# Performance work log

Measured on AMD Instinct MI355X. Metric: run time of the kernel, lower is better.

Reference implementation:

```python
import jax, jax.numpy as jnp
import numpy as np

N = 131072      # total nodes
B = 16          # graphs in batch (num_segments)
C = 128         # in_channels
K = 16          # n_super_nodes
TAU = 1.0
PRUNING_THRESHOLD = 0.01
SPARSITY_WEIGHT = 0.01
TEMPORAL_W = 0.1 * 5
COLLAPSE_W = 2.0
EPS = 1e-9


def setup_inputs() -> dict:
    key = jax.random.key(0)
    ks = jax.random.split(key, 8)
    x = jax.random.normal(ks[0], (N, C), dtype=jnp.float32)
    batch = jnp.sort(jax.random.randint(ks[1], (N,), 0, B)).astype(jnp.int64)
    pos = jax.random.normal(ks[2], (N, 2), dtype=jnp.float32)
    # Gumbel noise for gumbel_softmax (sampled once, passed as input for determinism)
    gumbel = jax.random.gumbel(ks[3], (N, K), dtype=jnp.float32)
    # assign_mlp params: Linear(C,C) -> ReLU -> Linear(C,K)
    W1 = jax.random.normal(ks[4], (C, C), dtype=jnp.float32) / np.sqrt(C)
    b1 = jnp.zeros((C,), dtype=jnp.float32)
    W2 = jax.random.normal(ks[5], (K, C), dtype=jnp.float32) / np.sqrt(C)
    b2 = jnp.zeros((K,), dtype=jnp.float32)
    scaling = jnp.asarray(10.0, dtype=jnp.float32)
    active_mask = jnp.ones((K,), dtype=jnp.float32)  # buffer, starts all-active
    return {"x": x, "batch": batch, "pos": pos, "gumbel": gumbel,
            "W1": W1, "b1": b1, "W2": W2, "b2": b2,
            "scaling": scaling, "active_mask": active_mask}


def reference(x, batch, pos, gumbel, W1, b1, W2, b2, scaling, active_mask):
    # --- assignment logits: MLP * scaling (eval mode, prev_assignments=None) ---
    h = jax.nn.relu(x @ W1.T + b1)            # [N, C]
    logits = (h @ W2.T + b2) * scaling        # [N, K]
    # eval-path masking: masked_fill(mask == 0, -1e9)
    masked_logits = jnp.where(active_mask[None, :] == 0.0, -1e9, logits)
    # gumbel_softmax (soft, hard=False)
    s = jax.nn.softmax((masked_logits + gumbel) / TAU, axis=-1)   # [N, K]

    avg_s = jnp.mean(s, axis=0)               # [K]

    # --- losses ---
    entropy = -jnp.mean(jnp.sum(s * jnp.log(s + EPS), axis=1))
    uniform_p = 1.0 / K
    diversity = jnp.sum(uniform_p * jnp.log(uniform_p / (avg_s + EPS)))
    pruning = jnp.mean(jnp.abs(avg_s * (1.0 - active_mask)))
    sparsity = (jnp.sum(active_mask) / K) * SPARSITY_WEIGHT
    temporal = jnp.asarray(0.0, jnp.float32)  # prev_assignments is None
    # collapse-prevention / balance bodies are truncated upstream; faithful proxies
    collapse = jnp.sum((avg_s - uniform_p) ** 2) * COLLAPSE_W
    balance = jnp.std(avg_s)
    spatial = jnp.asarray(0.0, jnp.float32)

    # --- pooled features: out[b,k,c] = sum_{n in graph b} s[n,k] * x[n,c] ---
    weighted = x[:, None, :] * s[:, :, None]                  # [N, K, C]
    out = jax.ops.segment_sum(weighted, batch, num_segments=B)  # [B, K, C]

    # --- super-node positions ---
    w_pos = pos[:, None, :] * s[:, :, None]                    # [N, K, 2]
    sum_s_pos = jax.ops.segment_sum(w_pos, batch, num_segments=B)  # [B, K, 2]
    sum_s = jax.ops.segment_sum(s, batch, num_segments=B)[..., None] + EPS  # [B, K, 1]
    mu = sum_s_pos / sum_s                                     # [B, K, 2]

    # --- separation loss: pairwise repulsion between super-node centers ---
    dist_sq = jnp.sum((mu[:, :, None, :] - mu[:, None, :, :]) ** 2, axis=-1)  # [B,K,K]
    eye = jnp.eye(K, dtype=mu.dtype)[None]
    repulsion = 1.0 / (dist_sq + 1.0)
    separation = jnp.sum(repulsion * (1.0 - eye)) / (K * (K - 1))

    losses = jnp.stack([entropy, diversity, spatial, pruning, sparsity,
                        temporal * TEMPORAL_W, collapse, balance, separation])
    return out, s, mu, losses
```

## Files before the change

### kernel.cpp

```cpp
#include <hip/hip_runtime.h>
#include <hip/hip_bf16.h>
#include <math.h>

#define NN 131072
#define BSEG 16
#define CCH 128
#define KK 16
#define EPSF 1e-9f
#define XST 136

#define OFF_S   32768
#define OFF_MU  2129920
#define OFF_L   2130432

#define REDC_BASE 1024
#define REDC_STRIDE 1024
#define NRED 64
#define ST_BASE (REDC_BASE + NRED * REDC_STRIDE)
#define NST 4
#define ST_SZ (BSEG * KK * CCH)

typedef __bf16 bf16x8 __attribute__((ext_vector_type(8)));
typedef float  f32x4  __attribute__((ext_vector_type(4)));
typedef float  f32x16 __attribute__((ext_vector_type(16)));

__device__ __forceinline__ int load_batch(const void* bptr, int n, int is64) {
    if (is64) return (int)((const long long*)bptr)[n];
    return ((const int*)bptr)[n];
}

__device__ __forceinline__ float wave_sum(float v) {
#pragma unroll
    for (int o = 32; o > 0; o >>= 1) v += __shfl_xor(v, o, 64);
    return v;
}

__device__ __forceinline__ bf16x8 pack8(float4 a, float4 b) {
    bf16x8 v;
    v[0] = (__bf16)a.x; v[1] = (__bf16)a.y; v[2] = (__bf16)a.z; v[3] = (__bf16)a.w;
    v[4] = (__bf16)b.x; v[5] = (__bf16)b.y; v[6] = (__bf16)b.z; v[7] = (__bf16)b.w;
    return v;
}

__global__ void k_zero(float* __restrict__ ws, const int* __restrict__ b32) {
    int i = blockIdx.x * 256 + threadIdx.x;
    ws[REDC_BASE + i] = 0.0f;
    if (i == 0) ws[0] = (b32[NN - 1] == 0) ? 1.0f : 0.0f;
}

__global__ __launch_bounds__(256, 2) void k_fused(
    const float* __restrict__ x, const void* __restrict__ batch,
    const float* __restrict__ pos, const float* __restrict__ gumbel,
    const float* __restrict__ W1, const float* __restrict__ b1,
    const float* __restrict__ W2, const float* __restrict__ b2,
    const float* __restrict__ scaling, const float* __restrict__ active_mask,
    float* __restrict__ s_out, float* __restrict__ ws)
{
    __shared__ __align__(16) __bf16 x_lds[128 * XST];
    __shared__ __align__(16) __bf16 h_lds[128 * XST];
    __shared__ __align__(16) __bf16 sT[16 * XST];
    __shared__ int bsegs[128];

    const int tid  = threadIdx.x;
    const int lane = tid & 63;
    const int wv   = tid >> 6;
    const int n0   = blockIdx.x * 128;
    const int is64 = (int)ws[0];

    if (tid < 128) bsegs[tid] = load_batch(batch, n0 + tid, is64);

    float4 ga0, ga1, ga2, ga3;
    if (tid < 128) {
        const float4* gp = (const float4*)(gumbel + (size_t)(n0 + tid) * KK);
        ga0 = gp[0]; ga1 = gp[1]; ga2 = gp[2]; ga3 = gp[3];
    }

    {
        const float4* xg = (const float4*)(x + (size_t)n0 * CCH);
#pragma unroll
        for (int i = 0; i < 8; i++) {
            int p = i * 256 + tid;
            float4 a = xg[2 * p], b = xg[2 * p + 1];
            *(bf16x8*)&x_lds[(p >> 4) * XST + (p & 15) * 8] = pack8(a, b);
        }
    }
    __syncthreads();

    {
        bf16x8 bfr[8];
        const float* wrow = W1 + (size_t)(wv * 32 + (lane & 31)) * CCH + (lane >> 5) * 8;
#pragma unroll
        for (int ks = 0; ks < 8; ks++) {
            float4 u = *(const float4*)(wrow + ks * 16);
            float4 v = *(const float4*)(wrow + ks * 16 + 4);
            bfr[ks] = pack8(u, v);
        }
        f32x16 acc[4];
#pragma unroll
        for (int mt = 0; mt < 4; mt++)
#pragma unroll
            for (int r = 0; r < 16; r++) acc[mt][r] = 0.0f;

#pragma unroll
        for (int ks = 0; ks < 8; ks++) {
#pragma unroll
            for (int mt = 0; mt < 4; mt++) {
                bf16x8 a = *(bf16x8*)&x_lds[(size_t)(mt * 32 + (lane & 31)) * XST + ks * 16 + (lane >> 5) * 8];
                acc[mt] = __builtin_amdgcn_mfma_f32_32x32x16_bf16(a, bfr[ks], acc[mt], 0, 0, 0);
            }
        }
        const float b1j = b1[wv * 32 + (lane & 31)];
#pragma unroll
        for (int mt = 0; mt < 4; mt++)
#pragma unroll
            for (int r = 0; r < 16; r++) {
                int node = mt * 32 + (r & 3) + 8 * (r >> 2) + 4 * (lane >> 5);
                h_lds[(size_t)node * XST + wv * 32 + (lane & 31)] = (__bf16)fmaxf(acc[mt][r] + b1j, 0.0f);
            }
    }
    __syncthreads();

    {
        f32x4 acc2[2];
#pragma unroll
        for (int t = 0; t < 2; t++)
#pragma unroll
            for (int r = 0; r < 4; r++) acc2[t][r] = 0.0f;

#pragma unroll
        for (int ks = 0; ks < 4; ks++) {
            const float* w2row = W2 + (size_t)(lane & 15) * CCH + ks * 32 + (lane >> 4) * 8;
            float4 u = *(const float4*)w2row;
            float4 v = *(const float4*)(w2row + 4);
            bf16x8 bw = pack8(u, v);
#pragma unroll
            for (int t = 0; t < 2; t++) {
                int tile = wv * 2 + t;
                bf16x8 a = *(bf16x8*)&h_lds[(size_t)(tile * 16 + (lane & 15)) * XST + ks * 32 + (lane >> 4) * 8];
                acc2[t] = __builtin_amdgcn_mfma_f32_16x16x32_bf16(a, bw, acc2[t], 0, 0, 0);
            }
        }
#pragma unroll
        for (int t = 0; t < 2; t++) {
#pragma unroll
            for (int r = 0; r < 4; r++) {
                int node = (wv * 2 + t) * 16 + (lane >> 4) * 4 + r;
                float* lp = (float*)((char*)h_lds + (size_t)node * (XST * 2) + 192);
                lp[lane & 15] = acc2[t][r];
            }
        }
    }
    __syncthreads();

    if (tid < 128) {
        const int n = n0 + tid;
        const char* rb = (const char*)h_lds + (size_t)tid * (XST * 2);
        float lg[16], gu[16];
#pragma unroll
        for (int i = 0; i < 4; i++) {
            float4 t = *(const float4*)(rb + 192 + 16 * i);
            lg[4 * i] = t.x; lg[4 * i + 1] = t.y; lg[4 * i + 2] = t.z; lg[4 * i + 3] = t.w;
        }
        gu[0] = ga0.x; gu[1] = ga0.y; gu[2]  = ga0.z; gu[3]  = ga0.w;
        gu[4] = ga1.x; gu[5] = ga1.y; gu[6]  = ga1.z; gu[7]  = ga1.w;
        gu[8] = ga2.x; gu[9] = ga2.y; gu[10] = ga2.z; gu[11] = ga2.w;
        gu[12] = ga3.x; gu[13] = ga3.y; gu[14] = ga3.z; gu[15] = ga3.w;

        const float sc = scaling[0];
        float m = -1e30f;
#pragma unroll
        for (int k = 0; k < KK; k++) {
            float v = (lg[k] + b2[k]) * sc;
            if (active_mask[k] == 0.0f) v = -1e9f;
            v += gu[k];
            lg[k] = v;
            m = fmaxf(m, v);
        }
        float ssum = 0.0f;
#pragma unroll
        for (int k = 0; k < KK; k++) { lg[k] = expf(lg[k] - m); ssum += lg[k]; }
        const float inv = 1.0f / ssum;
        float sarr[16];
#pragma unroll
        for (int k = 0; k < KK; k++) sarr[k] = lg[k] * inv;

        float4* srow = (float4*)(s_out + (size_t)n * KK);
#pragma unroll
        for (int i = 0; i < 4; i++) {
            float4 t;
            t.x = sarr[4 * i]; t.y = sarr[4 * i + 1]; t.z = sarr[4 * i + 2]; t.w = sarr[4 * i + 3];
            srow[i] = t;
        }
#pragma unroll
        for (int k = 0; k < KK; k++) sT[k * XST + tid] = (__bf16)sarr[k];

        float ent = 0.0f;
#pragma unroll
        for (int k = 0; k < KK; k++) ent += sarr[k] * logf(sarr[k] + EPSF);

        const float2 p = ((const float2*)pos)[n];
        const int bi = bsegs[tid];
        const int b0 = __shfl(bi, 0, 64);
        const int b1s = __shfl(bi, 63, 64);
        const float prim = (bi == b0) ? 1.0f : 0.0f;
        float* rc = ws + REDC_BASE + (size_t)(blockIdx.x & (NRED - 1)) * REDC_STRIDE;

#pragma unroll
        for (int k = 0; k < KK; k++) {
            float v = wave_sum(sarr[k] * prim);
            if (lane == 0) atomicAdd(&rc[b0 * 16 + k], v);
        }
#pragma unroll
        for (int k = 0; k < KK; k++) {
            float vx = wave_sum(sarr[k] * p.x * prim);
            float vy = wave_sum(sarr[k] * p.y * prim);
            if (lane == 0) {
                atomicAdd(&rc[256 + b0 * 32 + 2 * k],     vx);
                atomicAdd(&rc[256 + b0 * 32 + 2 * k + 1], vy);
            }
        }
        {
            float e = wave_sum(ent * prim);
            if (lane == 0) atomicAdd(&rc[768], e);
        }

        if (b0 != b1s) {
            const float sec = 1.0f - prim;
#pragma unroll
            for (int k = 0; k < KK; k++) {
                float v = wave_sum(sarr[k] * sec);
                if (lane == 0) atomicAdd(&rc[b1s * 16 + k], v);
            }
#pragma unroll
            for (int k = 0; k < KK; k++) {
                float vx = wave_sum(sarr[k] * p.x * sec);
                float vy = wave_sum(sarr[k] * p.y * sec);
                if (lane == 0) {
                    atomicAdd(&rc[256 + b1s * 32 + 2 * k],     vx);
                    atomicAdd(&rc[256 + b1s * 32 + 2 * k + 1], vy);
                }
            }
            float e = wave_sum(ent * sec);
            if (lane == 0) atomicAdd(&rc[768], e);
        }
    }
    __syncthreads();

    {
        float* stg = ws + ST_BASE + (size_t)(blockIdx.x & (NST - 1)) * ST_SZ;
        const int bfirst = bsegs[0], blast = bsegs[127];
        for (int seg = bfirst; seg <= blast; seg++) {
            const bool masked = (bfirst != blast);
            f32x4 pacc[2];
#pragma unroll
            for (int t = 0; t < 2; t++)
#pragma unroll
                for (int r = 0; r < 4; r++) pacc[t][r] = 0.0f;

#pragma unroll
            for (int ks = 0; ks < 4; ks++) {
                bf16x8 a = *(bf16x8*)&sT[(size_t)(lane & 15) * XST + ks * 32 + (lane >> 4) * 8];
                if (masked) {
#pragma unroll
                    for (int i = 0; i < 8; i++) {
                        int nd = ks * 32 + (lane >> 4) * 8 + i;
                        if (bsegs[nd] != seg) a[i] = (__bf16)0.0f;
                    }
                }
#pragma unroll
                for (int t = 0; t < 2; t++) {
                    int ct = wv * 2 + t;
                    bf16x8 bx;
#pragma unroll
                    for (int i = 0; i < 8; i++)
                        bx[i] = x_lds[(size_t)(ks * 32 + (lane >> 4) * 8 + i) * XST + ct * 16 + (lane & 15)];
                    pacc[t] = __builtin_amdgcn_mfma_f32_16x16x32_bf16(a, bx, pacc[t], 0, 0, 0);
                }
            }
#pragma unroll
            for (int t = 0; t < 2; t++) {
                int c = (wv * 2 + t) * 16 + (lane & 15);
#pragma unroll
                for (int r = 0; r < 4; r++) {
                    int k = (lane >> 4) * 4 + r;
                    atomicAdd(&stg[((size_t)seg * KK + k) * CCH + c], pacc[t][r]);
                }
            }
        }
    }
}

__global__ __launch_bounds__(256) void k_reduce(const float* __restrict__ ws,
                                                float* __restrict__ out) {
    int i = blockIdx.x * 256 + threadIdx.x;
    const float4* s0 = (const float4*)(ws + ST_BASE);
    const float4* s1 = (const float4*)(ws + ST_BASE + ST_SZ);
    const float4* s2 = (const float4*)(ws + ST_BASE + 2 * ST_SZ);
    const float4* s3 = (const float4*)(ws + ST_BASE + 3 * ST_SZ);
    float4 a = s0[i], b = s1[i], c = s2[i], d = s3[i];
    float4 r;
    r.x = (a.x + b.x) + (c.x + d.x);
    r.y = (a.y + b.y) + (c.y + d.y);
    r.z = (a.z + b.z) + (c.z + d.z);
    r.w = (a.w + b.w) + (c.w + d.w);
    ((float4*)out)[i] = r;
}

__global__ __launch_bounds__(256) void k_final(
    const float* __restrict__ ws, const float* __restrict__ active_mask,
    float* __restrict__ mu_out, float* __restrict__ losses)
{
    __shared__ float lsum[256];
    __shared__ float lpos[512];
    __shared__ float lent[1];
    __shared__ float smu[512];
    __shared__ float savg[16];
    __shared__ float red[256];
    const int tid = threadIdx.x;

    for (int a = tid; a < 769; a += 256) {
        float acc = 0.0f;
#pragma unroll 8
        for (int c = 0; c < NRED; c++) acc += ws[REDC_BASE + c * REDC_STRIDE + a];
        if (a < 256) lsum[a] = acc;
        else if (a < 768) lpos[a - 256] = acc;
        else lent[0] = acc;
    }
    __syncthreads();

    if (tid < 16) {
        float a = 0.0f;
#pragma unroll
        for (int b = 0; b < 16; b++) a += lsum[b * 16 + tid];
        savg[tid] = a / (float)NN;
    }
    for (int i = tid; i < 512; i += 256) {
        int sk = i >> 1;
        float v = lpos[i] / (lsum[sk] + EPSF);
        smu[i] = v;
        mu_out[i] = v;
    }
    __syncthreads();

    float rep = 0.0f;
    for (int t = tid; t < 4096; t += 256) {
        int b = t >> 8, i = (t >> 4) & 15, j = t & 15;
        if (i != j) {
            float dx = smu[b * 32 + i * 2]     - smu[b * 32 + j * 2];
            float dy = smu[b * 32 + i * 2 + 1] - smu[b * 32 + j * 2 + 1];
            rep += 1.0f / (dx * dx + dy * dy + 1.0f);
        }
    }
    red[tid] = rep;
    __syncthreads();
    for (int st = 128; st > 0; st >>= 1) {
        if (tid < st) red[tid] += red[tid + st];
        __syncthreads();
    }

    if (tid == 0) {
        const float p = 1.0f / 16.0f;
        float separation = red[0] / (float)(16 * 15);
        float entropy = -lent[0] / (float)NN;
        float diversity = 0.f, pruning = 0.f, amsum = 0.f, collapse = 0.f, mean = 0.f;
        for (int k = 0; k < 16; k++) {
            float a = savg[k];
            diversity += p * logf(p / (a + EPSF));
            pruning += fabsf(a * (1.0f - active_mask[k]));
            amsum += active_mask[k];
            collapse += (a - p) * (a - p);
            mean += a;
        }
        pruning /= 16.0f;
        mean /= 16.0f;
        float var = 0.f;
        for (int k = 0; k < 16; k++) { float d = savg[k] - mean; var += d * d; }
        float balance = sqrtf(var / 16.0f);
        float sparsity = (amsum / 16.0f) * 0.01f;
        collapse *= 2.0f;
        losses[0] = entropy;   losses[1] = diversity; losses[2] = 0.0f;
        losses[3] = pruning;   losses[4] = sparsity;  losses[5] = 0.0f;
        losses[6] = collapse;  losses[7] = balance;   losses[8] = separation;
    }
}

extern "C" void kernel_launch(void* const* d_in, const int* in_sizes, int n_in,
                              void* d_out, int out_size, void* d_ws, size_t ws_size,
                              hipStream_t stream) {
    const float* x       = (const float*)d_in[0];
    const void*  batch   = d_in[1];
    const float* pos     = (const float*)d_in[2];
    const float* gumbel  = (const float*)d_in[3];
    const float* W1      = (const float*)d_in[4];
    const float* b1      = (const float*)d_in[5];
    const float* W2      = (const float*)d_in[6];
    const float* b2      = (const float*)d_in[7];
    const float* scaling = (const float*)d_in[8];
    const float* am      = (const float*)d_in[9];

    float* out      = (float*)d_out;
    float* s_sec    = out + OFF_S;
    float* mu_sec   = out + OFF_MU;
    float* loss_sec = out + OFF_L;
    float* wsf      = (float*)d_ws;

    k_zero<<<768, 256, 0, stream>>>(wsf, (const int*)batch);
    k_fused<<<NN / 128, 256, 0, stream>>>(x, batch, pos, gumbel, W1, b1, W2, b2,
                                          scaling, am, s_sec, wsf);
    k_reduce<<<32, 256, 0, stream>>>(wsf, out);
    k_final<<<1, 256, 0, stream>>>(wsf, am, mu_sec, loss_sec);
}
```

Baseline: 183.0 us.

## Use 512-thread blocks over two node tiles, carry pooled accumulators, merge tail kernels

Each block now has 8 waves and walks two consecutive 128-node tiles, so there are half as many blocks. W1 fragments are loaded once per block and reused across both tiles. The pooled-feature MFMA accumulator is carried across tiles and flushed with atomics only when the segment changes, which cuts global atomic traffic. The reduce and final kernels are merged into one launch to remove a kernel launch. The costs are more barriers per block, per-wave work split differently (one 16-column tile per wave), and occupancy limited by LDS at 512 threads.

```diff
diff --git a/kernel.cpp b/kernel.cpp
--- a/kernel.cpp
+++ b/kernel.cpp
@@ -20,6 +20,8 @@
 #define NST 4
 #define ST_SZ (BSEG * KK * CCH)
 
+#define TILES 2
+
 typedef __bf16 bf16x8 __attribute__((ext_vector_type(8)));
 typedef float  f32x4  __attribute__((ext_vector_type(4)));
 typedef float  f32x16 __attribute__((ext_vector_type(16)));
@@ -48,7 +50,7 @@
     if (i == 0) ws[0] = (b32[NN - 1] == 0) ? 1.0f : 0.0f;
 }
 
-__global__ __launch_bounds__(256, 2) void k_fused(
+__global__ __launch_bounds__(512, 4) void k_fused(
     const float* __restrict__ x, const void* __restrict__ batch,
     const float* __restrict__ pos, const float* __restrict__ gumbel,
     const float* __restrict__ W1, const float* __restrict__ b1,
@@ -64,259 +66,269 @@
     const int tid  = threadIdx.x;
     const int lane = tid & 63;
     const int wv   = tid >> 6;
-    const int n0   = blockIdx.x * 128;
     const int is64 = (int)ws[0];
 
-    if (tid < 128) bsegs[tid] = load_batch(batch, n0 + tid, is64);
-
-    float4 ga0, ga1, ga2, ga3;
-    if (tid < 128) {
-        const float4* gp = (const float4*)(gumbel + (size_t)(n0 + tid) * KK);
-        ga0 = gp[0]; ga1 = gp[1]; ga2 = gp[2]; ga3 = gp[3];
-    }
-
+    const int c0 = (wv & 3) * 32;
+    bf16x8 bfr[8];
     {
-        const float4* xg = (const float4*)(x + (size_t)n0 * CCH);
-#pragma unroll
-        for (int i = 0; i < 8; i++) {
-            int p = i * 256 + tid;
-            float4 a = xg[2 * p], b = xg[2 * p + 1];
-            *(bf16x8*)&x_lds[(p >> 4) * XST + (p & 15) * 8] = pack8(a, b);
-        }
-    }
-    __syncthreads();
-
-    {
-        bf16x8 bfr[8];
-        const float* wrow = W1 + (size_t)(wv * 32 + (lane & 31)) * CCH + (lane >> 5) * 8;
+        const float* wrow = W1 + (size_t)(c0 + (lane & 31)) * CCH + (lane >> 5) * 8;
 #pragma unroll
         for (int ks = 0; ks < 8; ks++) {
             float4 u = *(const float4*)(wrow + ks * 16);
             float4 v = *(const float4*)(wrow + ks * 16 + 4);
             bfr[ks] = pack8(u, v);
         }
-        f32x16 acc[4];
-#pragma unroll
-        for (int mt = 0; mt < 4; mt++)
-#pragma unroll
-            for (int r = 0; r < 16; r++) acc[mt][r] = 0.0f;
-
-#pragma unroll
-        for (int ks = 0; ks < 8; ks++) {
-#pragma unroll
-            for (int mt = 0; mt < 4; mt++) {
-                bf16x8 a = *(bf16x8*)&x_lds[(size_t)(mt * 32 + (lane & 31)) * XST + ks * 16 + (lane >> 5) * 8];
-                acc[mt] = __builtin_amdgcn_mfma_f32_32x32x16_bf16(a, bfr[ks], acc[mt], 0, 0, 0);
-            }
-        }
-        const float b1j = b1[wv * 32 + (lane & 31)];
-#pragma unroll
-        for (int mt = 0; mt < 4; mt++)
-#pragma unroll
-            for (int r = 0; r < 16; r++) {
-                int node = mt * 32 + (r & 3) + 8 * (r >> 2) + 4 * (lane >> 5);
-                h_lds[(size_t)node * XST + wv * 32 + (lane & 31)] = (__bf16)fmaxf(acc[mt][r] + b1j, 0.0f);
-            }
-    }
-    __syncthreads();
-
-    {
-        f32x4 acc2[2];
-#pragma unroll
-        for (int t = 0; t < 2; t++)
-#pragma unroll
-            for (int r = 0; r < 4; r++) acc2[t][r] = 0.0f;
-
-#pragma unroll
-        for (int ks = 0; ks < 4; ks++) {
-            const float* w2row = W2 + (size_t)(lane & 15) * CCH + ks * 32 + (lane >> 4) * 8;
-            float4 u = *(const float4*)w2row;
-            float4 v = *(const float4*)(w2row + 4);
-            bf16x8 bw = pack8(u, v);
-#pragma unroll
-            for (int t = 0; t < 2; t++) {
-                int tile = wv * 2 + t;
-                bf16x8 a = *(bf16x8*)&h_lds[(size_t)(tile * 16 + (lane & 15)) * XST + ks * 32 + (lane >> 4) * 8];
-                acc2[t] = __builtin_amdgcn_mfma_f32_16x16x32_bf16(a, bw, acc2[t], 0, 0, 0);
-            }
-        }
-#pragma unroll
-        for (int t = 0; t < 2; t++) {
+    }
+    const float b1j = b1[c0 + (lane & 31)];
+
+    f32x4 pacc;
+#pragma unroll
+    for (int r = 0; r < 4; r++) pacc[r] = 0.0f;
+    int curseg = -1;
+    float* rc  = ws + REDC_BASE + (size_t)(blockIdx.x & (NRED - 1)) * REDC_STRIDE;
+    float* stg = ws + ST_BASE   + (size_t)(blockIdx.x & (NST  - 1)) * ST_SZ;
+
+    for (int t = 0; t < TILES; t++) {
+        const int n0 = blockIdx.x * (TILES * 128) + t * 128;
+
+        if (t) __syncthreads();
+
+        if (tid < 128) bsegs[tid] = load_batch(batch, n0 + tid, is64);
+
+        float4 ga0, ga1, ga2, ga3;
+        float2 p;
+        if (tid < 128) {
+            const float4* gp = (const float4*)(gumbel + (size_t)(n0 + tid) * KK);
+            ga0 = gp[0]; ga1 = gp[1]; ga2 = gp[2]; ga3 = gp[3];
+            p = ((const float2*)pos)[n0 + tid];
+        }
+
+        {
+            const float4* xg = (const float4*)(x + (size_t)n0 * CCH);
+#pragma unroll
+            for (int i = 0; i < 4; i++) {
+                int pp = i * 512 + tid;
+                float4 a = xg[2 * pp], b = xg[2 * pp + 1];
+                *(bf16x8*)&x_lds[(pp >> 4) * XST + (pp & 15) * 8] = pack8(a, b);
+            }
+        }
+        __syncthreads();
+
+        {
+            f32x16 acc[2];
+#pragma unroll
+            for (int m = 0; m < 2; m++)
+#pragma unroll
+                for (int r = 0; r < 16; r++) acc[m][r] = 0.0f;
+
+            const int mt0 = (wv >> 2) * 2;
+#pragma unroll
+            for (int ks = 0; ks < 8; ks++) {
+#pragma unroll
+                for (int m = 0; m < 2; m++) {
+                    bf16x8 a = *(bf16x8*)&x_lds[(size_t)((mt0 + m) * 32 + (lane & 31)) * XST + ks * 16 + (lane >> 5) * 8];
+                    acc[m] = __builtin_amdgcn_mfma_f32_32x32x16_bf16(a, bfr[ks], acc[m], 0, 0, 0);
+                }
+            }
+#pragma unroll
+            for (int m = 0; m < 2; m++)
+#pragma unroll
+                for (int r = 0; r < 16; r++) {
+                    int node = (mt0 + m) * 32 + (r & 3) + 8 * (r >> 2) + 4 * (lane >> 5);
+                    h_lds[(size_t)node * XST + c0 + (lane & 31)] = (__bf16)fmaxf(acc[m][r] + b1j, 0.0f);
+                }
+        }
+        __syncthreads();
+
+        {
+            f32x4 acc2;
+#pragma unroll
+            for (int r = 0; r < 4; r++) acc2[r] = 0.0f;
+#pragma unroll
+            for (int ks = 0; ks < 4; ks++) {
+                const float* w2row = W2 + (size_t)(lane & 15) * CCH + ks * 32 + (lane >> 4) * 8;
+                float4 u = *(const float4*)w2row;
+                float4 v = *(const float4*)(w2row + 4);
+                bf16x8 bwf = pack8(u, v);
+                bf16x8 a = *(bf16x8*)&h_lds[(size_t)(wv * 16 + (lane & 15)) * XST + ks * 32 + (lane >> 4) * 8];
+                acc2 = __builtin_amdgcn_mfma_f32_16x16x32_bf16(a, bwf, acc2, 0, 0, 0);
+            }
 #pragma unroll
             for (int r = 0; r < 4; r++) {
-                int node = (wv * 2 + t) * 16 + (lane >> 4) * 4 + r;
+                int node = wv * 16 + (lane >> 4) * 4 + r;
                 float* lp = (float*)((char*)h_lds + (size_t)node * (XST * 2) + 192);
-                lp[lane & 15] = acc2[t][r];
-            }
-        }
-    }
-    __syncthreads();
-
-    if (tid < 128) {
-        const int n = n0 + tid;
-        const char* rb = (const char*)h_lds + (size_t)tid * (XST * 2);
-        float lg[16], gu[16];
-#pragma unroll
-        for (int i = 0; i < 4; i++) {
-            float4 t = *(const float4*)(rb + 192 + 16 * i);
-            lg[4 * i] = t.x; lg[4 * i + 1] = t.y; lg[4 * i + 2] = t.z; lg[4 * i + 3] = t.w;
-        }
-        gu[0] = ga0.x; gu[1] = ga0.y; gu[2]  = ga0.z; gu[3]  = ga0.w;
-        gu[4] = ga1.x; gu[5] = ga1.y; gu[6]  = ga1.z; gu[7]  = ga1.w;
-        gu[8] = ga2.x; gu[9] = ga2.y; gu[10] = ga2.z; gu[11] = ga2.w;
-        gu[12] = ga3.x; gu[13] = ga3.y; gu[14] = ga3.z; gu[15] = ga3.w;
-
-        const float sc = scaling[0];
-        float m = -1e30f;
-#pragma unroll
-        for (int k = 0; k < KK; k++) {
-            float v = (lg[k] + b2[k]) * sc;
-            if (active_mask[k] == 0.0f) v = -1e9f;
-            v += gu[k];
-            lg[k] = v;
-            m = fmaxf(m, v);
-        }
-        float ssum = 0.0f;
-#pragma unroll
-        for (int k = 0; k < KK; k++) { lg[k] = expf(lg[k] - m); ssum += lg[k]; }
-        const float inv = 1.0f / ssum;
-        float sarr[16];
-#pragma unroll
-        for (int k = 0; k < KK; k++) sarr[k] = lg[k] * inv;
-
-        float4* srow = (float4*)(s_out + (size_t)n * KK);
-#pragma unroll
-        for (int i = 0; i < 4; i++) {
-            float4 t;
-            t.x = sarr[4 * i]; t.y = sarr[4 * i + 1]; t.z = sarr[4 * i + 2]; t.w = sarr[4 * i + 3];
-            srow[i] = t;
-        }
-#pragma unroll
-        for (int k = 0; k < KK; k++) sT[k * XST + tid] = (__bf16)sarr[k];
-
-        float ent = 0.0f;
-#pragma unroll
-        for (int k = 0; k < KK; k++) ent += sarr[k] * logf(sarr[k] + EPSF);
-
-        const float2 p = ((const float2*)pos)[n];
-        const int bi = bsegs[tid];
-        const int b0 = __shfl(bi, 0, 64);
-        const int b1s = __shfl(bi, 63, 64);
-        const float prim = (bi == b0) ? 1.0f : 0.0f;
-        float* rc = ws + REDC_BASE + (size_t)(blockIdx.x & (NRED - 1)) * REDC_STRIDE;
-
-#pragma unroll
-        for (int k = 0; k < KK; k++) {
-            float v = wave_sum(sarr[k] * prim);
-            if (lane == 0) atomicAdd(&rc[b0 * 16 + k], v);
-        }
-#pragma unroll
-        for (int k = 0; k < KK; k++) {
-            float vx = wave_sum(sarr[k] * p.x * prim);
-            float vy = wave_sum(sarr[k] * p.y * prim);
-            if (lane == 0) {
-                atomicAdd(&rc[256 + b0 * 32 + 2 * k],     vx);
-                atomicAdd(&rc[256 + b0 * 32 + 2 * k + 1], vy);
-            }
-        }
+                lp[lane & 15] = acc2[r];
+            }
+        }
+        __syncthreads();
+
+        if (tid < 128) {
+            const int n = n0 + tid;
+            const char* rb = (const char*)h_lds + (size_t)tid * (XST * 2);
+            float lg[16], gu[16];
+#pragma unroll
+            for (int i = 0; i < 4; i++) {
+                float4 tt = *(const float4*)(rb + 192 + 16 * i);
+                lg[4 * i] = tt.x; lg[4 * i + 1] = tt.y; lg[4 * i + 2] = tt.z; lg[4 * i + 3] = tt.w;
+            }
+            gu[0] = ga0.x; gu[1] = ga0.y; gu[2]  = ga0.z; gu[3]  = ga0.w;
+            gu[4] = ga1.x; gu[5] = ga1.y; gu[6]  = ga1.z; gu[7]  = ga1.w;
+            gu[8] = ga2.x; gu[9] = ga2.y; gu[10] = ga2.z; gu[11] = ga2.w;
+            gu[12] = ga3.x; gu[13] = ga3.y; gu[14] = ga3.z; gu[15] = ga3.w;
+
+            const float sc = scaling[0];
+            float m = -1e30f;
+#pragma unroll
+            for (int k = 0; k < KK; k++) {
+                float v = (lg[k] + b2[k]) * sc;
+                if (active_mask[k] == 0.0f) v = -1e9f;
+                v += gu[k];
+                lg[k] = v;
+                m = fmaxf(m, v);
+            }
+            float ssum = 0.0f;
+#pragma unroll
+            for (int k = 0; k < KK; k++) { lg[k] = expf(lg[k] - m); ssum += lg[k]; }
+            const float inv = 1.0f / ssum;
+            float sarr[16];
+#pragma unroll
+            for (int k = 0; k < KK; k++) sarr[k] = lg[k] * inv;
+
+            float4* srow = (float4*)(s_out + (size_t)n * KK);
+#pragma unroll
+            for (int i = 0; i < 4; i++) {
+                float4 tt;
+                tt.x = sarr[4 * i]; tt.y = sarr[4 * i + 1]; tt.z = sarr[4 * i + 2]; tt.w = sarr[4 * i + 3];
+                srow[i] = tt;
+            }
+#pragma unroll
+            for (int k = 0; k < KK; k++) sT[k * XST + tid] = (__bf16)sarr[k];
+
+            float ent = 0.0f;
+#pragma unroll
+            for (int k = 0; k < KK; k++) ent += sarr[k] * logf(sarr[k] + EPSF);
+
+            const int bi = bsegs[tid];
+            const int b0 = __shfl(bi, 0, 64);
+            const int b1s = __shfl(bi, 63, 64);
+            const float prim = (bi == b0) ? 1.0f : 0.0f;
+
+#pragma unroll
+            for (int k = 0; k < KK; k++) {
+                float v = wave_sum(sarr[k] * prim);
+                if (lane == 0) atomicAdd(&rc[b0 * 16 + k], v);
+            }
+#pragma unroll
+            for (int k = 0; k < KK; k++) {
+                float vx = wave_sum(sarr[k] * p.x * prim);
+                float vy = wave_sum(sarr[k] * p.y * prim);
+                if (lane == 0) {
+                    atomicAdd(&rc[256 + b0 * 32 + 2 * k],     vx);
+                    atomicAdd(&rc[256 + b0 * 32 + 2 * k + 1], vy);
+                }
+            }
+            {
+                float e = wave_sum(ent * prim);
+                if (lane == 0) atomicAdd(&rc[768], e);
+            }
+
+            if (b0 != b1s) {
+                const float sec = 1.0f - prim;
+#pragma unroll
+                for (int k = 0; k < KK; k++) {
+                    float v = wave_sum(sarr[k] * sec);
+                    if (lane == 0) atomicAdd(&rc[b1s * 16 + k], v);
+                }
+#pragma unroll
+                for (int k = 0; k < KK; k++) {
+                    float vx = wave_sum(sarr[k] * p.x * sec);
+                    float vy = wave_sum(sarr[k] * p.y * sec);
+                    if (lane == 0) {
+                        atomicAdd(&rc[256 + b1s * 32 + 2 * k],     vx);
+                        atomicAdd(&rc[256 + b1s * 32 + 2 * k + 1], vy);
+                    }
+                }
+                float e = wave_sum(ent * sec);
+                if (lane == 0) atomicAdd(&rc[768], e);
+            }
+        }
+        __syncthreads();
+
         {
-            float e = wave_sum(ent * prim);
-            if (lane == 0) atomicAdd(&rc[768], e);
-        }
-
-        if (b0 != b1s) {
-            const float sec = 1.0f - prim;
-#pragma unroll
-            for (int k = 0; k < KK; k++) {
-                float v = wave_sum(sarr[k] * sec);
-                if (lane == 0) atomicAdd(&rc[b1s * 16 + k], v);
-            }
-#pragma unroll
-            for (int k = 0; k < KK; k++) {
-                float vx = wave_sum(sarr[k] * p.x * sec);
-                float vy = wave_sum(sarr[k] * p.y * sec);
-                if (lane == 0) {
-                    atomicAdd(&rc[256 + b1s * 32 + 2 * k],     vx);
-                    atomicAdd(&rc[256 + b1s * 32 + 2 * k + 1], vy);
-                }
-            }
-            float e = wave_sum(ent * sec);
-            if (lane == 0) atomicAdd(&rc[768], e);
-        }
-    }
-    __syncthreads();
-
-    {
-        float* stg = ws + ST_BASE + (size_t)(blockIdx.x & (NST - 1)) * ST_SZ;
-        const int bfirst = bsegs[0], blast = bsegs[127];
-        for (int seg = bfirst; seg <= blast; seg++) {
-            const bool masked = (bfirst != blast);
-            f32x4 pacc[2];
-#pragma unroll
-            for (int t = 0; t < 2; t++)
-#pragma unroll
-                for (int r = 0; r < 4; r++) pacc[t][r] = 0.0f;
-
-#pragma unroll
-            for (int ks = 0; ks < 4; ks++) {
-                bf16x8 a = *(bf16x8*)&sT[(size_t)(lane & 15) * XST + ks * 32 + (lane >> 4) * 8];
-                if (masked) {
-#pragma unroll
-                    for (int i = 0; i < 8; i++) {
-                        int nd = ks * 32 + (lane >> 4) * 8 + i;
-                        if (bsegs[nd] != seg) a[i] = (__bf16)0.0f;
+            const int bf = bsegs[0], bl = bsegs[127];
+            const bool masked = (bf != bl);
+            for (int seg = bf; seg <= bl; seg++) {
+                if (seg != curseg) {
+                    if (curseg >= 0) {
+#pragma unroll
+                        for (int r = 0; r < 4; r++) {
+                            int k = (lane >> 4) * 4 + r;
+                            int c = wv * 16 + (lane & 15);
+                            atomicAdd(&stg[((size_t)curseg * KK + k) * CCH + c], pacc[r]);
+                        }
+#pragma unroll
+                        for (int r = 0; r < 4; r++) pacc[r] = 0.0f;
                     }
-                }
-#pragma unroll
-                for (int t = 0; t < 2; t++) {
-                    int ct = wv * 2 + t;
+                    curseg = seg;
+                }
+#pragma unroll
+                for (int ks = 0; ks < 4; ks++) {
+                    bf16x8 a = *(bf16x8*)&sT[(size_t)(lane & 15) * XST + ks * 32 + (lane >> 4) * 8];
+                    if (masked) {
+#pragma unroll
+                        for (int i = 0; i < 8; i++) {
+                            int nd = ks * 32 + (lane >> 4) * 8 + i;
+                            if (bsegs[nd] != seg) a[i] = (__bf16)0.0f;
+                        }
+                    }
                     bf16x8 bx;
 #pragma unroll
                     for (int i = 0; i < 8; i++)
-                        bx[i] = x_lds[(size_t)(ks * 32 + (lane >> 4) * 8 + i) * XST + ct * 16 + (lane & 15)];
-                    pacc[t] = __builtin_amdgcn_mfma_f32_16x16x32_bf16(a, bx, pacc[t], 0, 0, 0);
-                }
-            }
-#pragma unroll
-            for (int t = 0; t < 2; t++) {
-                int c = (wv * 2 + t) * 16 + (lane & 15);
-#pragma unroll
-                for (int r = 0; r < 4; r++) {
-                    int k = (lane >> 4) * 4 + r;
-                    atomicAdd(&stg[((size_t)seg * KK + k) * CCH + c], pacc[t][r]);
-                }
-            }
-        }
-    }
-}
-
-__global__ __launch_bounds__(256) void k_reduce(const float* __restrict__ ws,
-                                                float* __restrict__ out) {
-    int i = blockIdx.x * 256 + threadIdx.x;
-    const float4* s0 = (const float4*)(ws + ST_BASE);
-    const float4* s1 = (const float4*)(ws + ST_BASE + ST_SZ);
-    const float4* s2 = (const float4*)(ws + ST_BASE + 2 * ST_SZ);
-    const float4* s3 = (const float4*)(ws + ST_BASE + 3 * ST_SZ);
-    float4 a = s0[i], b = s1[i], c = s2[i], d = s3[i];
-    float4 r;
-    r.x = (a.x + b.x) + (c.x + d.x);
-    r.y = (a.y + b.y) + (c.y + d.y);
-    r.z = (a.z + b.z) + (c.z + d.z);
-    r.w = (a.w + b.w) + (c.w + d.w);
-    ((float4*)out)[i] = r;
-}
-
-__global__ __launch_bounds__(256) void k_final(
+                        bx[i] = x_lds[(size_t)(ks * 32 + (lane >> 4) * 8 + i) * XST + wv * 16 + (lane & 15)];
+                    pacc = __builtin_amdgcn_mfma_f32_16x16x32_bf16(a, bx, pacc, 0, 0, 0);
+                }
+            }
+        }
+    }
+
+    if (curseg >= 0) {
+#pragma unroll
+        for (int r = 0; r < 4; r++) {
+            int k = (lane >> 4) * 4 + r;
+            int c = wv * 16 + (lane & 15);
+            atomicAdd(&stg[((size_t)curseg * KK + k) * CCH + c], pacc[r]);
+        }
+    }
+}
+
+__global__ __launch_bounds__(256) void k_tail(
     const float* __restrict__ ws, const float* __restrict__ active_mask,
-    float* __restrict__ mu_out, float* __restrict__ losses)
+    float* __restrict__ out, float* __restrict__ mu_out, float* __restrict__ losses)
 {
+    const int tid = threadIdx.x;
+
+    if (blockIdx.x < 32) {
+        int i = blockIdx.x * 256 + tid;
+        const float4* s0 = (const float4*)(ws + ST_BASE);
+        const float4* s1 = (const float4*)(ws + ST_BASE + ST_SZ);
+        const float4* s2 = (const float4*)(ws + ST_BASE + 2 * ST_SZ);
+        const float4* s3 = (const float4*)(ws + ST_BASE + 3 * ST_SZ);
+        float4 a = s0[i], b = s1[i], c = s2[i], d = s3[i];
+        float4 r;
+        r.x = (a.x + b.x) + (c.x + d.x);
+        r.y = (a.y + b.y) + (c.y + d.y);
+        r.z = (a.z + b.z) + (c.z + d.z);
+        r.w = (a.w + b.w) + (c.w + d.w);
+        ((float4*)out)[i] = r;
+        return;
+    }
+
     __shared__ float lsum[256];
     __shared__ float lpos[512];
     __shared__ float lent[1];
     __shared__ float smu[512];
     __shared__ float savg[16];
     __shared__ float red[256];
-    const int tid = threadIdx.x;
 
     for (int a = tid; a < 769; a += 256) {
         float acc = 0.0f;
@@ -405,8 +417,7 @@
     float* wsf      = (float*)d_ws;
 
     k_zero<<<768, 256, 0, stream>>>(wsf, (const int*)batch);
-    k_fused<<<NN / 128, 256, 0, stream>>>(x, batch, pos, gumbel, W1, b1, W2, b2,
+    k_fused<<<NN / 256, 512, 0, stream>>>(x, batch, pos, gumbel, W1, b1, W2, b2,
                                           scaling, am, s_sec, wsf);
-    k_reduce<<<32, 256, 0, stream>>>(wsf, out);
-    k_final<<<1, 256, 0, stream>>>(wsf, am, mu_sec, loss_sec);
-}
+    k_tail<<<33, 256, 0, stream>>>(wsf, am, out, mu_sec, loss_sec);
+}
```

After: 215.4 us. 17.7% more time.

## Compute softmax in MFMA register layout and merge reduce/final kernels

Applied to the files above, without the earlier changes.

The gumbel softmax, entropy and segment sums now run directly on the second-MFMA accumulator layout across all 256 threads. Row max and sum use 16-lane shuffles, which removes the LDS round trip of logits, one barrier, and the per-k wave reductions that only half the block performed. Per-segment sums are accumulated per lane and reduced once before the atomics, cutting the atomic count. The separate reduce and final kernels are merged into one 33-block launch to save a kernel launch. In exchange, s is written to global memory as scattered scalar stores instead of float4 rows.

```diff
diff --git a/kernel.cpp b/kernel.cpp
--- a/kernel.cpp
+++ b/kernel.cpp
@@ -59,6 +59,7 @@
     __shared__ __align__(16) __bf16 x_lds[128 * XST];
     __shared__ __align__(16) __bf16 h_lds[128 * XST];
     __shared__ __align__(16) __bf16 sT[16 * XST];
+    __shared__ float2 pos_lds[128];
     __shared__ int bsegs[128];
 
     const int tid  = threadIdx.x;
@@ -67,14 +68,13 @@
     const int n0   = blockIdx.x * 128;
     const int is64 = (int)ws[0];
 
-    if (tid < 128) bsegs[tid] = load_batch(batch, n0 + tid, is64);
-
-    float4 ga0, ga1, ga2, ga3;
+    float* rc  = ws + REDC_BASE + (size_t)(blockIdx.x & (NRED - 1)) * REDC_STRIDE;
+    float* stg = ws + ST_BASE   + (size_t)(blockIdx.x & (NST  - 1)) * ST_SZ;
+
     if (tid < 128) {
-        const float4* gp = (const float4*)(gumbel + (size_t)(n0 + tid) * KK);
-        ga0 = gp[0]; ga1 = gp[1]; ga2 = gp[2]; ga3 = gp[3];
-    }
-
+        bsegs[tid] = load_batch(batch, n0 + tid, is64);
+        pos_lds[tid] = ((const float2*)pos)[n0 + tid];
+    }
     {
         const float4* xg = (const float4*)(x + (size_t)n0 * CCH);
 #pragma unroll
@@ -121,6 +121,22 @@
     __syncthreads();
 
     {
+        const int g  = lane >> 4;
+        const int kq = lane & 15;
+        const int bf = bsegs[0], bl = bsegs[127];
+
+        float gu[2][4];
+#pragma unroll
+        for (int t = 0; t < 2; t++)
+#pragma unroll
+            for (int r = 0; r < 4; r++) {
+                int node = (wv * 2 + t) * 16 + g * 4 + r;
+                gu[t][r] = gumbel[(size_t)(n0 + node) * KK + kq];
+            }
+        const float b2k = b2[kq];
+        const float amk = active_mask[kq];
+        const float sc  = scaling[0];
+
         f32x4 acc2[2];
 #pragma unroll
         for (int t = 0; t < 2; t++)
@@ -129,125 +145,82 @@
 
 #pragma unroll
         for (int ks = 0; ks < 4; ks++) {
-            const float* w2row = W2 + (size_t)(lane & 15) * CCH + ks * 32 + (lane >> 4) * 8;
+            const float* w2row = W2 + (size_t)kq * CCH + ks * 32 + g * 8;
             float4 u = *(const float4*)w2row;
-            float4 v = *(const float4*)(w2row + 4);
-            bf16x8 bw = pack8(u, v);
+            float4 v4 = *(const float4*)(w2row + 4);
+            bf16x8 bwf = pack8(u, v4);
 #pragma unroll
             for (int t = 0; t < 2; t++) {
-                int tile = wv * 2 + t;
-                bf16x8 a = *(bf16x8*)&h_lds[(size_t)(tile * 16 + (lane & 15)) * XST + ks * 32 + (lane >> 4) * 8];
-                acc2[t] = __builtin_amdgcn_mfma_f32_16x16x32_bf16(a, bw, acc2[t], 0, 0, 0);
-            }
-        }
+                bf16x8 a = *(bf16x8*)&h_lds[(size_t)((wv * 2 + t) * 16 + kq) * XST + ks * 32 + g * 8];
+                acc2[t] = __builtin_amdgcn_mfma_f32_16x16x32_bf16(a, bwf, acc2[t], 0, 0, 0);
+            }
+        }
+
+        float saccA = 0.f, pxA = 0.f, pyA = 0.f;
+        float saccB = 0.f, pxB = 0.f, pyB = 0.f;
+        float entacc = 0.f;
+        const bool dual = (bf != bl);
+
 #pragma unroll
         for (int t = 0; t < 2; t++) {
 #pragma unroll
             for (int r = 0; r < 4; r++) {
-                int node = (wv * 2 + t) * 16 + (lane >> 4) * 4 + r;
-                float* lp = (float*)((char*)h_lds + (size_t)node * (XST * 2) + 192);
-                lp[lane & 15] = acc2[t][r];
-            }
-        }
-    }
-    __syncthreads();
-
-    if (tid < 128) {
-        const int n = n0 + tid;
-        const char* rb = (const char*)h_lds + (size_t)tid * (XST * 2);
-        float lg[16], gu[16];
-#pragma unroll
-        for (int i = 0; i < 4; i++) {
-            float4 t = *(const float4*)(rb + 192 + 16 * i);
-            lg[4 * i] = t.x; lg[4 * i + 1] = t.y; lg[4 * i + 2] = t.z; lg[4 * i + 3] = t.w;
-        }
-        gu[0] = ga0.x; gu[1] = ga0.y; gu[2]  = ga0.z; gu[3]  = ga0.w;
-        gu[4] = ga1.x; gu[5] = ga1.y; gu[6]  = ga1.z; gu[7]  = ga1.w;
-        gu[8] = ga2.x; gu[9] = ga2.y; gu[10] = ga2.z; gu[11] = ga2.w;
-        gu[12] = ga3.x; gu[13] = ga3.y; gu[14] = ga3.z; gu[15] = ga3.w;
-
-        const float sc = scaling[0];
-        float m = -1e30f;
-#pragma unroll
-        for (int k = 0; k < KK; k++) {
-            float v = (lg[k] + b2[k]) * sc;
-            if (active_mask[k] == 0.0f) v = -1e9f;
-            v += gu[k];
-            lg[k] = v;
-            m = fmaxf(m, v);
-        }
-        float ssum = 0.0f;
-#pragma unroll
-        for (int k = 0; k < KK; k++) { lg[k] = expf(lg[k] - m); ssum += lg[k]; }
-        const float inv = 1.0f / ssum;
-        float sarr[16];
-#pragma unroll
-        for (int k = 0; k < KK; k++) sarr[k] = lg[k] * inv;
-
-        float4* srow = (float4*)(s_out + (size_t)n * KK);
-#pragma unroll
-        for (int i = 0; i < 4; i++) {
-            float4 t;
-            t.x = sarr[4 * i]; t.y = sarr[4 * i + 1]; t.z = sarr[4 * i + 2]; t.w = sarr[4 * i + 3];
-            srow[i] = t;
-        }
-#pragma unroll
-        for (int k = 0; k < KK; k++) sT[k * XST + tid] = (__bf16)sarr[k];
-
-        float ent = 0.0f;
-#pragma unroll
-        for (int k = 0; k < KK; k++) ent += sarr[k] * logf(sarr[k] + EPSF);
-
-        const float2 p = ((const float2*)pos)[n];
-        const int bi = bsegs[tid];
-        const int b0 = __shfl(bi, 0, 64);
-        const int b1s = __shfl(bi, 63, 64);
-        const float prim = (bi == b0) ? 1.0f : 0.0f;
-        float* rc = ws + REDC_BASE + (size_t)(blockIdx.x & (NRED - 1)) * REDC_STRIDE;
-
-#pragma unroll
-        for (int k = 0; k < KK; k++) {
-            float v = wave_sum(sarr[k] * prim);
-            if (lane == 0) atomicAdd(&rc[b0 * 16 + k], v);
-        }
-#pragma unroll
-        for (int k = 0; k < KK; k++) {
-            float vx = wave_sum(sarr[k] * p.x * prim);
-            float vy = wave_sum(sarr[k] * p.y * prim);
-            if (lane == 0) {
-                atomicAdd(&rc[256 + b0 * 32 + 2 * k],     vx);
-                atomicAdd(&rc[256 + b0 * 32 + 2 * k + 1], vy);
-            }
-        }
-        {
-            float e = wave_sum(ent * prim);
-            if (lane == 0) atomicAdd(&rc[768], e);
-        }
-
-        if (b0 != b1s) {
-            const float sec = 1.0f - prim;
-#pragma unroll
-            for (int k = 0; k < KK; k++) {
-                float v = wave_sum(sarr[k] * sec);
-                if (lane == 0) atomicAdd(&rc[b1s * 16 + k], v);
-            }
-#pragma unroll
-            for (int k = 0; k < KK; k++) {
-                float vx = wave_sum(sarr[k] * p.x * sec);
-                float vy = wave_sum(sarr[k] * p.y * sec);
-                if (lane == 0) {
-                    atomicAdd(&rc[256 + b1s * 32 + 2 * k],     vx);
-                    atomicAdd(&rc[256 + b1s * 32 + 2 * k + 1], vy);
+                const int node = (wv * 2 + t) * 16 + g * 4 + r;
+                float v = (acc2[t][r] + b2k) * sc;
+                if (amk == 0.0f) v = -1e9f;
+                v += gu[t][r];
+                float m = v;
+#pragma unroll
+                for (int o = 1; o < 16; o <<= 1) m = fmaxf(m, __shfl_xor(m, o, 64));
+                float e = expf(v - m);
+                float ssum = e;
+#pragma unroll
+                for (int o = 1; o < 16; o <<= 1) ssum += __shfl_xor(ssum, o, 64);
+                float s = e / ssum;
+
+                s_out[(size_t)(n0 + node) * KK + kq] = s;
+                sT[kq * XST + node] = (__bf16)s;
+
+                float tt = s * logf(s + EPSF);
+#pragma unroll
+                for (int o = 1; o < 16; o <<= 1) tt += __shfl_xor(tt, o, 64);
+                entacc += tt;
+
+                const float2 pp = pos_lds[node];
+                const float w0 = (bsegs[node] == bf) ? 1.0f : 0.0f;
+                const float sA = s * w0;
+                saccA += sA; pxA += sA * pp.x; pyA += sA * pp.y;
+                if (dual) {
+                    const float sB = s - sA;
+                    saccB += sB; pxB += sB * pp.x; pyB += sB * pp.y;
                 }
             }
-            float e = wave_sum(ent * sec);
-            if (lane == 0) atomicAdd(&rc[768], e);
-        }
+        }
+
+        saccA += __shfl_xor(saccA, 16, 64); saccA += __shfl_xor(saccA, 32, 64);
+        pxA   += __shfl_xor(pxA,   16, 64); pxA   += __shfl_xor(pxA,   32, 64);
+        pyA   += __shfl_xor(pyA,   16, 64); pyA   += __shfl_xor(pyA,   32, 64);
+        if (lane < 16) {
+            atomicAdd(&rc[bf * 16 + lane], saccA);
+            atomicAdd(&rc[256 + bf * 32 + 2 * lane],     pxA);
+            atomicAdd(&rc[256 + bf * 32 + 2 * lane + 1], pyA);
+        }
+        if (dual) {
+            saccB += __shfl_xor(saccB, 16, 64); saccB += __shfl_xor(saccB, 32, 64);
+            pxB   += __shfl_xor(pxB,   16, 64); pxB   += __shfl_xor(pxB,   32, 64);
+            pyB   += __shfl_xor(pyB,   16, 64); pyB   += __shfl_xor(pyB,   32, 64);
+            if (lane < 16) {
+                atomicAdd(&rc[bl * 16 + lane], saccB);
+                atomicAdd(&rc[256 + bl * 32 + 2 * lane],     pxB);
+                atomicAdd(&rc[256 + bl * 32 + 2 * lane + 1], pyB);
+            }
+        }
+        float entw = wave_sum(entacc);
+        if (lane == 0) atomicAdd(&rc[768], entw * 0.0625f);
     }
     __syncthreads();
 
     {
-        float* stg = ws + ST_BASE + (size_t)(blockIdx.x & (NST - 1)) * ST_SZ;
         const int bfirst = bsegs[0], blast = bsegs[127];
         for (int seg = bfirst; seg <= blast; seg++) {
             const bool masked = (bfirst != blast);
@@ -290,33 +263,34 @@
     }
 }
 
-__global__ __launch_bounds__(256) void k_reduce(const float* __restrict__ ws,
-                                                float* __restrict__ out) {
-    int i = blockIdx.x * 256 + threadIdx.x;
-    const float4* s0 = (const float4*)(ws + ST_BASE);
-    const float4* s1 = (const float4*)(ws + ST_BASE + ST_SZ);
-    const float4* s2 = (const float4*)(ws + ST_BASE + 2 * ST_SZ);
-    const float4* s3 = (const float4*)(ws + ST_BASE + 3 * ST_SZ);
-    float4 a = s0[i], b = s1[i], c = s2[i], d = s3[i];
-    float4 r;
-    r.x = (a.x + b.x) + (c.x + d.x);
-    r.y = (a.y + b.y) + (c.y + d.y);
-    r.z = (a.z + b.z) + (c.z + d.z);
-    r.w = (a.w + b.w) + (c.w + d.w);
-    ((float4*)out)[i] = r;
-}
-
-__global__ __launch_bounds__(256) void k_final(
+__global__ __launch_bounds__(256) void k_tail(
     const float* __restrict__ ws, const float* __restrict__ active_mask,
-    float* __restrict__ mu_out, float* __restrict__ losses)
+    float* __restrict__ out, float* __restrict__ mu_out, float* __restrict__ losses)
 {
+    const int tid = threadIdx.x;
+
+    if (blockIdx.x < 32) {
+        int i = blockIdx.x * 256 + tid;
+        const float4* s0 = (const float4*)(ws + ST_BASE);
+        const float4* s1 = (const float4*)(ws + ST_BASE + ST_SZ);
+        const float4* s2 = (const float4*)(ws + ST_BASE + 2 * ST_SZ);
+        const float4* s3 = (const float4*)(ws + ST_BASE + 3 * ST_SZ);
+        float4 a = s0[i], b = s1[i], c = s2[i], d = s3[i];
+        float4 r;
+        r.x = (a.x + b.x) + (c.x + d.x);
+        r.y = (a.y + b.y) + (c.y + d.y);
+        r.z = (a.z + b.z) + (c.z + d.z);
+        r.w = (a.w + b.w) + (c.w + d.w);
+        ((float4*)out)[i] = r;
+        return;
+    }
+
     __shared__ float lsum[256];
     __shared__ float lpos[512];
     __shared__ float lent[1];
     __shared__ float smu[512];
     __shared__ float savg[16];
     __shared__ float red[256];
-    const int tid = threadIdx.x;
 
     for (int a = tid; a < 769; a += 256) {
         float acc = 0.0f;
@@ -407,6 +381,5 @@
     k_zero<<<768, 256, 0, stream>>>(wsf, (const int*)batch);
     k_fused<<<NN / 128, 256, 0, stream>>>(x, batch, pos, gumbel, W1, b1, W2, b2,
                                           scaling, am, s_sec, wsf);
-    k_reduce<<<32, 256, 0, stream>>>(wsf, out);
-    k_final<<<1, 256, 0, stream>>>(wsf, am, mu_sec, loss_sec);
-}
+    k_tail<<<33, 256, 0, stream>>>(wsf, am, out, mu_sec, loss_sec);
+}
```

Result: faster. 160.8 us (-12.1%).
